# Kernel tuning notes

Hardware: AMD Instinct MI355X
Metric: run time of the kernel (lower is better)

The kernel has to match this reference:

```python
import jax, jax.numpy as jnp
import numpy as np

E = 512       # embed_dim
H = 8         # num_heads
DH = E // H   # head dim
F = 2048      # dim_feedforward
KS = 33       # NATTEN kernel_size (dilation=1)
NCLS = 1
B = 2
L = 4096      # local tokens (total seq = L + NCLS)
EPS = 1e-5


def layernorm(x, g, b):
    mu = jnp.mean(x, axis=-1, keepdims=True)
    var = jnp.mean(jnp.square(x - mu), axis=-1, keepdims=True)
    return (x - mu) * jax.lax.rsqrt(var + EPS) * g + b


def natten_1d(x, qkv_w, qkv_b, proj_w, proj_b):
    # Neighborhood attention 1D, dilation=1, non-causal, no rel-pos bias.
    b, l, e = x.shape
    qkv = x @ qkv_w.T + qkv_b                       # [b, l, 3E]
    q, k, v = jnp.split(qkv, 3, axis=-1)
    q = q.reshape(b, l, H, DH) * (DH ** -0.5)
    k = k.reshape(b, l, H, DH)
    v = v.reshape(b, l, H, DH)
    # NATTEN window: centered, shifted at edges to keep exactly KS in-bounds neighbors
    starts = jnp.clip(jnp.arange(l) - KS // 2, 0, l - KS)   # [l]
    idx = starts[:, None] + jnp.arange(KS)                  # [l, KS]
    kn = k[:, idx]                                          # [b, l, KS, H, DH]
    vn = v[:, idx]                                          # [b, l, KS, H, DH]
    attn = jnp.einsum('blhd,blkhd->bhlk', q, kn)
    attn = jax.nn.softmax(attn, axis=-1)
    out = jnp.einsum('bhlk,blkhd->blhd', attn, vn).reshape(b, l, e)
    return out @ proj_w.T + proj_b


def global_mha(q_in, kv_in, in_w, in_b, out_w, out_b):
    # torch nn.MultiheadAttention, batch_first, no masks
    bq, lq, e = q_in.shape
    lk = kv_in.shape[1]
    wq, wk, wv = jnp.split(in_w, 3, axis=0)
    bqp, bkp, bvp = jnp.split(in_b, 3, axis=0)
    q = (q_in @ wq.T + bqp).reshape(bq, lq, H, DH) * (DH ** -0.5)
    k = (kv_in @ wk.T + bkp).reshape(bq, lk, H, DH)
    v = (kv_in @ wv.T + bvp).reshape(bq, lk, H, DH)
    attn = jax.nn.softmax(jnp.einsum('bqhd,bkhd->bhqk', q, k), axis=-1)
    out = jnp.einsum('bhqk,bkhd->bqhd', attn, v).reshape(bq, lq, e)
    return out @ out_w.T + out_b


def setup_inputs() -> dict:
    key = jax.random.key(0)
    ks = jax.random.split(key, 16)
    s = 0.02
    return {
        'x': jax.random.normal(ks[0], (B, L + NCLS, E), jnp.float32),
        'ln1_g': jnp.ones((E,), jnp.float32),
        'ln1_b': jnp.zeros((E,), jnp.float32),
        'qkv_w': jax.random.normal(ks[1], (3 * E, E), jnp.float32) * s,
        'qkv_b': jnp.zeros((3 * E,), jnp.float32),
        'na_proj_w': jax.random.normal(ks[2], (E, E), jnp.float32) * s,
        'na_proj_b': jnp.zeros((E,), jnp.float32),
        'in_proj_w': jax.random.normal(ks[3], (3 * E, E), jnp.float32) * s,
        'in_proj_b': jnp.zeros((3 * E,), jnp.float32),
        'out_w': jax.random.normal(ks[4], (E, E), jnp.float32) * s,
        'out_b': jnp.zeros((E,), jnp.float32),
        'ln2_g': jnp.ones((E,), jnp.float32),
        'ln2_b': jnp.zeros((E,), jnp.float32),
        'fc1_w': jax.random.normal(ks[5], (F, E), jnp.float32) * s,
        'fc1_b': jnp.zeros((F,), jnp.float32),
        'fc2_w': jax.random.normal(ks[6], (E, F), jnp.float32) * s,
        'fc2_b': jnp.zeros((E,), jnp.float32),
    }


def reference(x, ln1_g, ln1_b, qkv_w, qkv_b, na_proj_w, na_proj_b,
              in_proj_w, in_proj_b, out_w, out_b, ln2_g, ln2_b,
              fc1_w, fc1_b, fc2_w, fc2_b):
    res = x
    xn = layernorm(x, ln1_g, ln1_b)
    x_local = natten_1d(xn[:, :-NCLS, :], qkv_w, qkv_b, na_proj_w, na_proj_b)
    tmp_key = jnp.concatenate([x_local, xn[:, -NCLS:, :]], axis=1)
    x_cls = global_mha(xn[:, -NCLS:, :], tmp_key, in_proj_w, in_proj_b, out_w, out_b)
    x = res + jnp.concatenate([x_local, x_cls], axis=1)
    res = x
    xn = layernorm(x, ln2_g, ln2_b)
    h = jax.nn.silu(xn @ fc1_w.T + fc1_b)
    return res + (h @ fc2_w.T + fc2_b)
```

## Files before the change

kernel.cpp:

```cpp
#include <hip/hip_runtime.h>
#include <hip/hip_bf16.h>
#include <cstdint>
#include <cstddef>

#define E    512
#define H    8
#define DHD  64
#define FDIM 2048
#define KS   33
#define BB   2
#define LL   4096
#define LP1  4097
#define NTOK 8194
#define NLOC 8192

typedef unsigned short ushort_t;
typedef __bf16 bf16x8_t __attribute__((ext_vector_type(8)));
typedef float  f32x4_t  __attribute__((ext_vector_type(4)));

__device__ __forceinline__ float b2f(unsigned short h) {
  union { unsigned int u; float f; } un; un.u = ((unsigned int)h) << 16; return un.f;
}
__device__ __forceinline__ unsigned short f2b(float f) {
  union { float f; unsigned int u; } un; un.f = f;
  unsigned int u = un.u;
  return (unsigned short)((u + 0x7FFFu + ((u >> 16) & 1u)) >> 16);
}

__device__ __forceinline__ void gload16(const ushort_t* g, ushort_t* l) {
  __builtin_amdgcn_global_load_lds(
      (const __attribute__((address_space(1))) void*)g,
      (__attribute__((address_space(3))) void*)l,
      16, 0, 0);
}

template<int N> __device__ __forceinline__ void waitcnt_vm() {
  if constexpr (N == 8)      asm volatile("s_waitcnt vmcnt(8)" ::: "memory");
  else if constexpr (N == 6) asm volatile("s_waitcnt vmcnt(6)" ::: "memory");
  else                       asm volatile("s_waitcnt vmcnt(0)" ::: "memory");
}

__device__ __forceinline__ int xcd_remap(int hw, int n) {
  int xcd = hw & 7, j = hw >> 3;
  int q = n >> 3, r = n & 7;
  return (xcd < r ? xcd * (q + 1) : r * (q + 1) + (xcd - r) * q) + j;
}

template<int BNT, int WC, int ACT, int OUTF, int ADDRES, int INRM, int OUTRM, int PARTIAL>
__global__ __launch_bounds__(256) void gemm_bt(
    const ushort_t* __restrict__ A, const ushort_t* __restrict__ W,
    const float* __restrict__ bias, float* __restrict__ outF,
    ushort_t* __restrict__ outB, const float* __restrict__ res,
    int M, int N, int K, int klen, int ny, int nz, size_t pstr)
{
  constexpr int MF  = 4;
  constexpr int NF  = BNT / (WC * 16);
  constexpr int BR  = (BNT * 64) / (8 * 256);
  constexpr int NLD = 4 + BR;
  __shared__ ushort_t Alds[2][128 * 64];
  __shared__ ushort_t Blds[2][BNT * 64];
  const int t    = threadIdx.x;
  const int lane = t & 63;
  const int w    = t >> 6;
  const int wr   = w / WC, wc = w % WC;

  const int Lid = xcd_remap(blockIdx.x, gridDim.x);
  const int bx  = Lid / (ny * nz);
  const int rem = Lid % (ny * nz);
  const int z   = rem / ny;
  const int by  = rem % ny;
  const int bmBase = bx * 128;
  const int bnBase = by * BNT;
  const int kbeg = z * klen;

  f32x4_t zero = {0.f, 0.f, 0.f, 0.f};
  f32x4_t acc[MF][NF];
  #pragma unroll
  for (int m = 0; m < MF; ++m)
    #pragma unroll
    for (int n = 0; n < NF; ++n) acc[m][n] = zero;

  const int srow = t >> 3;
  const int jsw8 = ((t & 7) ^ (srow & 7)) * 8;
  int arow[4];
  #pragma unroll
  for (int r = 0; r < 4; ++r) {
    int rr = bmBase + r * 32 + srow;
    if (INRM) rr += rr >> 12;
    else if (rr >= M) rr = M - 1;
    arow[r] = rr;
  }
  int brow[BR];
  #pragma unroll
  for (int r = 0; r < BR; ++r) brow[r] = bnBase + r * 32 + srow;

  const int frow = lane & 15;
  const int g    = lane >> 4;

  auto STAGE = [&](int s, int k0) {
    #pragma unroll
    for (int r = 0; r < 4; ++r)
      gload16(A + (size_t)arow[r] * K + k0 + jsw8, &Alds[s][(size_t)(r * 256 + t) * 8]);
    #pragma unroll
    for (int r = 0; r < BR; ++r)
      gload16(W + (size_t)brow[r] * K + k0 + jsw8, &Blds[s][(size_t)(r * 256 + t) * 8]);
  };

  const int nt = klen >> 6;
  STAGE(0, kbeg);
  if (nt > 1) STAGE(1, kbeg + 64);

  for (int it = 0; it < nt; ++it) {
    const int cur = it & 1;
    if (it < nt - 1) waitcnt_vm<NLD>();
    else             waitcnt_vm<0>();
    __builtin_amdgcn_s_barrier();
    #pragma unroll
    for (int kk2 = 0; kk2 < 2; ++kk2) {
      bf16x8_t af[MF], bfv[NF];
      const int kosw = ((kk2 * 4 + g) ^ (frow & 7)) << 4;
      #pragma unroll
      for (int m = 0; m < MF; ++m) {
        int row = wr * 64 + m * 16 + frow;
        af[m] = *reinterpret_cast<const bf16x8_t*>((char*)Alds[cur] + row * 128 + kosw);
      }
      #pragma unroll
      for (int n = 0; n < NF; ++n) {
        int row = wc * (BNT / WC) + n * 16 + frow;
        bfv[n] = *reinterpret_cast<const bf16x8_t*>((char*)Blds[cur] + row * 128 + kosw);
      }
      __builtin_amdgcn_s_setprio(1);
      #pragma unroll
      for (int m = 0; m < MF; ++m)
        #pragma unroll
        for (int n = 0; n < NF; ++n)
          acc[m][n] = __builtin_amdgcn_mfma_f32_16x16x32_bf16(af[m], bfv[n], acc[m][n], 0, 0, 0);
      __builtin_amdgcn_s_setprio(0);
    }
    __builtin_amdgcn_s_barrier();
    if (it + 2 < nt) STAGE(cur, kbeg + (it + 2) * 64);
  }

  const int rbase = g * 4;
  const int cbase = frow;
  float* po = nullptr;
  if (PARTIAL) po = (z == nz - 1) ? (float*)outB : outF + (size_t)z * pstr;
  #pragma unroll
  for (int m = 0; m < MF; ++m) {
    #pragma unroll
    for (int r = 0; r < 4; ++r) {
      int gr = bmBase + wr * 64 + m * 16 + rbase + r;
      if (gr < M) {
        int orow = OUTRM ? gr + (gr >> 12) : gr;
        #pragma unroll
        for (int n = 0; n < NF; ++n) {
          int gc = bnBase + wc * (BNT / WC) + n * 16 + cbase;
          float v = acc[m][n][r];
          if (PARTIAL) {
            po[(size_t)orow * N + gc] = v;
          } else {
            v += bias[gc];
            if (ACT == 1) v = v / (1.f + __expf(-v));
            if (ADDRES) v += res[(size_t)gr * N + gc];
            if (OUTF) outF[(size_t)orow * N + gc] = v;
            else      outB[(size_t)orow * N + gc] = f2b(v);
          }
        }
      }
    }
  }
}

template<int NP>
__global__ __launch_bounds__(256) void fc2_reduce(
    float* __restrict__ out, const float* __restrict__ parts, size_t pstr4,
    const float* __restrict__ bias, const float* __restrict__ xa)
{
  size_t i = (size_t)blockIdx.x * 256 + threadIdx.x;
  float4 o = reinterpret_cast<const float4*>(out)[i];
  float4 x = reinterpret_cast<const float4*>(xa)[i];
  float4 bcol = reinterpret_cast<const float4*>(bias)[i & 127];
  o.x += x.x + bcol.x; o.y += x.y + bcol.y;
  o.z += x.z + bcol.z; o.w += x.w + bcol.w;
  #pragma unroll
  for (int zp = 0; zp < NP - 1; ++zp) {
    float4 a = reinterpret_cast<const float4*>(parts)[zp * pstr4 + i];
    o.x += a.x; o.y += a.y; o.z += a.z; o.w += a.w;
  }
  reinterpret_cast<float4*>(out)[i] = o;
}

__global__ __launch_bounds__(256) void ln_fused1(
    const float* __restrict__ x, const float* __restrict__ g,
    const float* __restrict__ be, ushort_t* __restrict__ xn,
    ushort_t* __restrict__ tmpk)
{
  __shared__ float sh[4];
  const int row = blockIdx.x;
  const int t = threadIdx.x;
  const float* xr = x + (size_t)row * E;
  float v0 = xr[t], v1 = xr[t + 256];
  float sum = v0 + v1;
  #pragma unroll
  for (int o = 32; o; o >>= 1) sum += __shfl_xor(sum, o);
  if ((t & 63) == 0) sh[t >> 6] = sum;
  __syncthreads();
  float mean = (sh[0] + sh[1] + sh[2] + sh[3]) * (1.f / E);
  __syncthreads();
  float d0 = v0 - mean, d1 = v1 - mean;
  float vs = d0 * d0 + d1 * d1;
  #pragma unroll
  for (int o = 32; o; o >>= 1) vs += __shfl_xor(vs, o);
  if ((t & 63) == 0) sh[t >> 6] = vs;
  __syncthreads();
  float var = (sh[0] + sh[1] + sh[2] + sh[3]) * (1.f / E);
  float rstd = rsqrtf(var + 1e-5f);
  unsigned short o0 = f2b(d0 * rstd * g[t] + be[t]);
  unsigned short o1 = f2b(d1 * rstd * g[t + 256] + be[t + 256]);
  xn[(size_t)row * E + t] = o0;
  xn[(size_t)row * E + t + 256] = o1;
  if ((row % LP1) == LL) {
    tmpk[(size_t)row * E + t] = o0;
    tmpk[(size_t)row * E + t + 256] = o1;
  }
}

__global__ __launch_bounds__(256) void resid_ln2(
    const float* __restrict__ x, const ushort_t* __restrict__ tmpk,
    const float* __restrict__ xcls, const float* __restrict__ g,
    const float* __restrict__ be, float* __restrict__ xa,
    ushort_t* __restrict__ xn2)
{
  __shared__ float sh[4];
  const int row = blockIdx.x;
  const int b = row / LP1, l = row % LP1;
  const int t = threadIdx.x;
  float a0, a1;
  if (l < LL) { a0 = b2f(tmpk[(size_t)row * E + t]); a1 = b2f(tmpk[(size_t)row * E + t + 256]); }
  else        { a0 = xcls[b * E + t];                a1 = xcls[b * E + t + 256]; }
  float v0 = x[(size_t)row * E + t] + a0;
  float v1 = x[(size_t)row * E + t + 256] + a1;
  xa[(size_t)row * E + t] = v0;
  xa[(size_t)row * E + t + 256] = v1;
  float sum = v0 + v1;
  #pragma unroll
  for (int o = 32; o; o >>= 1) sum += __shfl_xor(sum, o);
  if ((t & 63) == 0) sh[t >> 6] = sum;
  __syncthreads();
  float mean = (sh[0] + sh[1] + sh[2] + sh[3]) * (1.f / E);
  __syncthreads();
  float d0 = v0 - mean, d1 = v1 - mean;
  float vs = d0 * d0 + d1 * d1;
  #pragma unroll
  for (int o = 32; o; o >>= 1) vs += __shfl_xor(vs, o);
  if ((t & 63) == 0) sh[t >> 6] = vs;
  __syncthreads();
  float var = (sh[0] + sh[1] + sh[2] + sh[3]) * (1.f / E);
  float rstd = rsqrtf(var + 1e-5f);
  xn2[(size_t)row * E + t]       = f2b(d0 * rstd * g[t] + be[t]);
  xn2[(size_t)row * E + t + 256] = f2b(d1 * rstd * g[t + 256] + be[t + 256]);
}

__global__ __launch_bounds__(256) void natten_mfma(
    const ushort_t* __restrict__ qkv, ushort_t* __restrict__ out)
{
  __shared__ ushort_t KP[4][64 * 64];
  __shared__ ushort_t VT[4][64 * 72];
  const int w    = threadIdx.x >> 6;
  const int lane = threadIdx.x & 63;
  const int task = blockIdx.x * 4 + w;
  const int h  = task & 7;
  const int qb = (task >> 3) & 127;
  const int b  = task >> 10;
  const int l0 = qb * 32;
  const int kb = l0 - 16;
  const ushort_t* base = qkv + (size_t)b * LL * (3 * E);
  ushort_t* Klds = KP[w];
  ushort_t* Vt   = VT[w];

  {
    const int rsub = lane >> 3;
    const int d0   = (lane & 7) * 8;
    #pragma unroll
    for (int i = 0; i < 8; ++i) {
      int row = i * 8 + rsub;
      int gl = kb + row; gl = gl < 0 ? 0 : (gl > LL - 1 ? LL - 1 : gl);
      bf16x8_t kv = *reinterpret_cast<const bf16x8_t*>(
          base + (size_t)gl * (3 * E) + E + h * 64 + d0);
      int ba = (row * 128 + d0 * 2) ^ ((row & 7) << 4);
      *reinterpret_cast<bf16x8_t*>((char*)Klds + ba) = kv;
    }
  }
  {
    const int a  = lane & 7;
    const int c8 = lane >> 3;
    unsigned int* Vt32 = (unsigned int*)Vt;
    #pragma unroll
    for (int i = 0; i < 4; ++i) {
      int rp = i * 8 + c8;
      int g0 = kb + rp * 2;     g0 = g0 < 0 ? 0 : (g0 > LL - 1 ? LL - 1 : g0);
      int g1 = kb + rp * 2 + 1; g1 = g1 < 0 ? 0 : (g1 > LL - 1 ? LL - 1 : g1);
      const ushort_t* v0 = base + (size_t)g0 * (3 * E) + 2 * E + h * 64 + a * 8;
      const ushort_t* v1 = base + (size_t)g1 * (3 * E) + 2 * E + h * 64 + a * 8;
      ushort4 x0 = *(const ushort4*)v0,       x1 = *(const ushort4*)v1;
      ushort4 y0 = *(const ushort4*)(v0 + 4), y1 = *(const ushort4*)(v1 + 4);
      int d = a * 8;
      Vt32[(d + 0) * 36 + rp] = (unsigned)x0.x | ((unsigned)x1.x << 16);
      Vt32[(d + 1) * 36 + rp] = (unsigned)x0.y | ((unsigned)x1.y << 16);
      Vt32[(d + 2) * 36 + rp] = (unsigned)x0.z | ((unsigned)x1.z << 16);
      Vt32[(d + 3) * 36 + rp] = (unsigned)x0.w | ((unsigned)x1.w << 16);
      Vt32[(d + 4) * 36 + rp] = (unsigned)y0.x | ((unsigned)y1.x << 16);
      Vt32[(d + 5) * 36 + rp] = (unsigned)y0.y | ((unsigned)y1.y << 16);
      Vt32[(d + 6) * 36 + rp] = (unsigned)y0.z | ((unsigned)y1.z << 16);
      Vt32[(d + 7) * 36 + rp] = (unsigned)y0.w | ((unsigned)y1.w << 16);
    }
  }

  const int p = lane & 15, g = lane >> 4;
  bf16x8_t qf[2][2];
  #pragma unroll
  for (int mt = 0; mt < 2; ++mt)
    #pragma unroll
    for (int ks = 0; ks < 2; ++ks)
      qf[mt][ks] = *reinterpret_cast<const bf16x8_t*>(
          base + (size_t)(l0 + mt * 16 + p) * (3 * E) + h * 64 + ks * 32 + g * 8);

  f32x4_t zero = {0.f, 0.f, 0.f, 0.f};
  f32x4_t accS[2][4];
  #pragma unroll
  for (int mt = 0; mt < 2; ++mt)
    #pragma unroll
    for (int nt = 0; nt < 4; ++nt) accS[mt][nt] = zero;
  #pragma unroll
  for (int ks = 0; ks < 2; ++ks) {
    bf16x8_t kf[4];
    #pragma unroll
    for (int nt = 0; nt < 4; ++nt) {
      int row = nt * 16 + p;
      int ba = (row * 128 + (ks * 32 + g * 8) * 2) ^ ((row & 7) << 4);
      kf[nt] = *reinterpret_cast<const bf16x8_t*>((char*)Klds + ba);
    }
    #pragma unroll
    for (int mt = 0; mt < 2; ++mt)
      #pragma unroll
      for (int nt = 0; nt < 4; ++nt)
        accS[mt][nt] = __builtin_amdgcn_mfma_f32_16x16x32_bf16(qf[mt][ks], kf[nt], accS[mt][nt], 0, 0, 0);
  }

  ushort_t* Plds = Klds;
  #pragma unroll
  for (int mt = 0; mt < 2; ++mt) {
    #pragma unroll
    for (int r = 0; r < 4; ++r) {
      int lq = l0 + mt * 16 + g * 4 + r;
      int st = lq - 16; st = st < 0 ? 0 : (st > LL - KS ? LL - KS : st);
      int clo = st - kb, chi = clo + 32;
      float sv[4];
      float mx = -1e30f;
      #pragma unroll
      for (int nt = 0; nt < 4; ++nt) {
        int c = nt * 16 + p;
        float s = accS[mt][nt][r] * 0.125f;
        s = (c >= clo && c <= chi) ? s : -1e30f;
        sv[nt] = s;
        mx = fmaxf(mx, s);
      }
      mx = fmaxf(mx, __shfl_xor(mx, 1));
      mx = fmaxf(mx, __shfl_xor(mx, 2));
      mx = fmaxf(mx, __shfl_xor(mx, 4));
      mx = fmaxf(mx, __shfl_xor(mx, 8));
      float sum = 0.f;
      #pragma unroll
      for (int nt = 0; nt < 4; ++nt) { float e = __expf(sv[nt] - mx); sv[nt] = e; sum += e; }
      sum += __shfl_xor(sum, 1);
      sum += __shfl_xor(sum, 2);
      sum += __shfl_xor(sum, 4);
      sum += __shfl_xor(sum, 8);
      float inv = 1.f / sum;
      int q = mt * 16 + g * 4 + r;
      #pragma unroll
      for (int nt = 0; nt < 4; ++nt)
        Plds[q * 72 + nt * 16 + p] = f2b(sv[nt] * inv);
    }
  }

  f32x4_t accO[2][4];
  #pragma unroll
  for (int mt = 0; mt < 2; ++mt)
    #pragma unroll
    for (int nt = 0; nt < 4; ++nt) accO[mt][nt] = zero;
  #pragma unroll
  for (int ks = 0; ks < 2; ++ks) {
    bf16x8_t pf[2], vf[4];
    #pragma unroll
    for (int mt = 0; mt < 2; ++mt)
      pf[mt] = *reinterpret_cast<const bf16x8_t*>(
          (char*)Plds + (mt * 16 + p) * 144 + (ks * 32 + g * 8) * 2);
    #pragma unroll
    for (int nt = 0; nt < 4; ++nt)
      vf[nt] = *reinterpret_cast<const bf16x8_t*>(
          (char*)Vt + (nt * 16 + p) * 144 + (ks * 32 + g * 8) * 2);
    #pragma unroll
    for (int mt = 0; mt < 2; ++mt)
      #pragma unroll
      for (int nt = 0; nt < 4; ++nt)
        accO[mt][nt] = __builtin_amdgcn_mfma_f32_16x16x32_bf16(pf[mt], vf[nt], accO[mt][nt], 0, 0, 0);
  }

  #pragma unroll
  for (int mt = 0; mt < 2; ++mt) {
    #pragma unroll
    for (int r = 0; r < 4; ++r) {
      int lq = l0 + mt * 16 + g * 4 + r;
      ushort_t* orow = out + ((size_t)(b * LL) + lq) * E + h * 64;
      #pragma unroll
      for (int nt = 0; nt < 4; ++nt)
        orow[nt * 16 + p] = f2b(accO[mt][nt][r]);
    }
  }
}

__global__ __launch_bounds__(256) void qcls_kernel(
    const ushort_t* __restrict__ xn, const float* __restrict__ inw,
    const float* __restrict__ inb, float* __restrict__ qcls)
{
  int i = blockIdx.x * 256 + threadIdx.x;
  int b = i >> 9, d = i & 511;
  const ushort_t* xr = xn + ((size_t)b * LP1 + LL) * E;
  const float* wr = inw + (size_t)d * E;
  float s = 0.f;
  for (int e = 0; e < E; e += 4) {
    ushort4 xv = *reinterpret_cast<const ushort4*>(xr + e);
    s += b2f(xv.x) * wr[e] + b2f(xv.y) * wr[e + 1] + b2f(xv.z) * wr[e + 2] + b2f(xv.w) * wr[e + 3];
  }
  qcls[i] = (s + inb[d]) * 0.125f;
}

__global__ __launch_bounds__(256) void gscore_kernel(
    const float* __restrict__ qcls, const ushort_t* __restrict__ kv,
    float* __restrict__ sc)
{
  const int wav = blockIdx.x * 4 + (threadIdx.x >> 6);
  if (wav >= BB * LP1) return;
  const int lane = threadIdx.x & 63;
  const int b = wav / LP1, j = wav % LP1;
  const ushort_t* kr = kv + (size_t)wav * 1024 + lane * 8;
  const float* q = qcls + b * E + lane * 8;
  ushort4 ka = *reinterpret_cast<const ushort4*>(kr);
  ushort4 kb4 = *reinterpret_cast<const ushort4*>(kr + 4);
  float s = b2f(ka.x) * q[0] + b2f(ka.y) * q[1] + b2f(ka.z) * q[2] + b2f(ka.w) * q[3]
          + b2f(kb4.x) * q[4] + b2f(kb4.y) * q[5] + b2f(kb4.z) * q[6] + b2f(kb4.w) * q[7];
  s += __shfl_xor(s, 1); s += __shfl_xor(s, 2); s += __shfl_xor(s, 4);
  if ((lane & 7) == 0) sc[((size_t)(b * 8) + (lane >> 3)) * LP1 + j] = s;
}

__global__ __launch_bounds__(256) void gsoftmax_kernel(float* __restrict__ sc)
{
  float* row = sc + (size_t)blockIdx.x * LP1;
  __shared__ float sh[4];
  const int t = threadIdx.x;
  float m = -1e30f;
  for (int i = t; i < LP1; i += 256) m = fmaxf(m, row[i]);
  #pragma unroll
  for (int o = 32; o; o >>= 1) m = fmaxf(m, __shfl_xor(m, o));
  if ((t & 63) == 0) sh[t >> 6] = m;
  __syncthreads();
  m = fmaxf(fmaxf(sh[0], sh[1]), fmaxf(sh[2], sh[3]));
  __syncthreads();
  float s = 0.f;
  for (int i = t; i < LP1; i += 256) { float e = __expf(row[i] - m); row[i] = e; s += e; }
  #pragma unroll
  for (int o = 32; o; o >>= 1) s += __shfl_xor(s, o);
  if ((t & 63) == 0) sh[t >> 6] = s;
  __syncthreads();
  float inv = 1.f / (sh[0] + sh[1] + sh[2] + sh[3]);
  for (int i = t; i < LP1; i += 256) row[i] *= inv;
}

__global__ __launch_bounds__(256) void gpv_kernel(
    const float* __restrict__ sc, const ushort_t* __restrict__ kv,
    float* __restrict__ parts)
{
  __shared__ float red[4][64];
  const int bh = blockIdx.y;
  const int b = bh >> 3, h = bh & 7;
  const int c = blockIdx.x;
  const int lane = threadIdx.x & 63, s4 = threadIdx.x >> 6;
  const int j0 = c * 512;
  const int jend = (j0 + 512 < LP1) ? j0 + 512 : LP1;
  const float* prow = sc + (size_t)bh * LP1;
  const ushort_t* vbase = kv + (size_t)b * LP1 * 1024 + 512 + h * 64 + lane;
  float acc = 0.f;
  for (int j = j0 + s4; j < jend; j += 4)
    acc += prow[j] * b2f(vbase[(size_t)j * 1024]);
  red[s4][lane] = acc;
  __syncthreads();
  if (s4 == 0)
    parts[((size_t)c * 16 + bh) * 64 + lane] = red[0][lane] + red[1][lane] + red[2][lane] + red[3][lane];
}

__global__ void gpv_reduce(const float* __restrict__ parts, float* __restrict__ oc)
{
  int i = blockIdx.x * 256 + threadIdx.x;
  if (i < BB * E) {
    float s = 0.f;
    #pragma unroll
    for (int c = 0; c < 9; ++c) s += parts[c * 1024 + i];
    oc[i] = s;
  }
}

__global__ __launch_bounds__(256) void xcls_kernel(
    const float* __restrict__ oc, const float* __restrict__ ow,
    const float* __restrict__ ob, float* __restrict__ xc)
{
  int i = blockIdx.x * 256 + threadIdx.x;
  if (i >= BB * E) return;
  int b = i >> 9, n = i & 511;
  const float* o = oc + b * E;
  const float* wr = ow + (size_t)n * E;
  float s = ob[n];
  for (int m = 0; m < E; ++m) s += o[m] * wr[m];
  xc[i] = s;
}

__global__ void cvt_all(
    const float* __restrict__ s0, ushort_t* __restrict__ d0, int n0,
    const float* __restrict__ s1, ushort_t* __restrict__ d1, int n1,
    const float* __restrict__ s2, ushort_t* __restrict__ d2, int n2,
    const float* __restrict__ s3, ushort_t* __restrict__ d3, int n3,
    const float* __restrict__ s4, ushort_t* __restrict__ d4, int n4)
{
  int i = (blockIdx.x * 256 + threadIdx.x) * 4;
  const float* s; ushort_t* d;
  if (i < n0)                { s = s0; d = d0; }
  else if ((i -= n0) < n1)   { s = s1; d = d1; }
  else if ((i -= n1) < n2)   { s = s2; d = d2; }
  else if ((i -= n2) < n3)   { s = s3; d = d3; }
  else if ((i -= n3) < n4)   { s = s4; d = d4; }
  else return;
  float4 v = *reinterpret_cast<const float4*>(s + i);
  ushort4 o;
  o.x = f2b(v.x); o.y = f2b(v.y); o.z = f2b(v.z); o.w = f2b(v.w);
  *reinterpret_cast<ushort4*>(d + i) = o;
}

extern "C" void kernel_launch(void* const* d_in, const int* in_sizes, int n_in,
                              void* d_out, int out_size, void* d_ws, size_t ws_size,
                              hipStream_t stream)
{
  const float* x      = (const float*)d_in[0];
  const float* ln1_g  = (const float*)d_in[1];
  const float* ln1_b  = (const float*)d_in[2];
  const float* qkv_w  = (const float*)d_in[3];
  const float* qkv_b  = (const float*)d_in[4];
  const float* na_w   = (const float*)d_in[5];
  const float* na_b   = (const float*)d_in[6];
  const float* in_w   = (const float*)d_in[7];
  const float* in_b   = (const float*)d_in[8];
  const float* out_w  = (const float*)d_in[9];
  const float* out_b  = (const float*)d_in[10];
  const float* ln2_g  = (const float*)d_in[11];
  const float* ln2_b  = (const float*)d_in[12];
  const float* fc1_w  = (const float*)d_in[13];
  const float* fc1_b  = (const float*)d_in[14];
  const float* fc2_w  = (const float*)d_in[15];
  const float* fc2_b  = (const float*)d_in[16];
  float* out = (float*)d_out;

  char* pws = (char*)d_ws;
  size_t off = 0;
  auto alloc = [&](size_t bytes) {
    void* r = pws + off; off = (off + bytes + 255) & ~(size_t)255; return r;
  };
  ushort_t* w_qkv = (ushort_t*)alloc((size_t)3 * E * E * 2);
  ushort_t* w_na  = (ushort_t*)alloc((size_t)E * E * 2);
  ushort_t* w_in  = (ushort_t*)alloc((size_t)3 * E * E * 2);
  ushort_t* w_fc1 = (ushort_t*)alloc((size_t)FDIM * E * 2);
  ushort_t* w_fc2 = (ushort_t*)alloc((size_t)E * FDIM * 2);
  ushort_t* xn1   = (ushort_t*)alloc((size_t)NTOK * E * 2);
  char*     bigR  = (char*)alloc((size_t)NTOK * FDIM * 2);
  ushort_t* qkvb  = (ushort_t*)bigR;
  ushort_t* natt  = (ushort_t*)(bigR + (size_t)NLOC * 3 * E * 2);
  ushort_t* kvg   = (ushort_t*)bigR;
  ushort_t* hbuf  = (ushort_t*)bigR;
  ushort_t* tmpk  = (ushort_t*)alloc((size_t)NTOK * E * 2);
  float*    sc    = (float*)alloc((size_t)BB * H * LP1 * 4);
  float*    qcls  = (float*)alloc(1024 * 4);
  float*    parts = (float*)alloc(9 * 16 * 64 * 4);
  float*    oc    = (float*)alloc(1024 * 4);
  float*    xcls  = (float*)alloc(1024 * 4);
  float*    xa    = (float*)alloc((size_t)NTOK * E * 4);
  ushort_t* xn2   = xn1;
  const size_t PS = (size_t)NTOK * E;
  size_t off_save = off;
  float* sk = (float*)alloc(3 * PS * 4);
  int nsplit = 4;
  if (off > ws_size) {
    off = off_save;
    sk = (float*)alloc(PS * 4);
    nsplit = 2;
    if (off > ws_size) { off = off_save; nsplit = 1; }
  }

  cvt_all<<<3840, 256, 0, stream>>>(
      qkv_w, w_qkv, 3 * E * E,
      na_w,  w_na,  E * E,
      in_w,  w_in,  3 * E * E,
      fc1_w, w_fc1, FDIM * E,
      fc2_w, w_fc2, E * FDIM);

  ln_fused1<<<NTOK, 256, 0, stream>>>(x, ln1_g, ln1_b, xn1, tmpk);
  qcls_kernel<<<4, 256, 0, stream>>>(xn1, in_w, in_b, qcls);
  gemm_bt<128,2, 0,0,0,1,0,0><<<64 * 12, 256, 0, stream>>>(
      xn1, w_qkv, qkv_b, nullptr, qkvb, nullptr, NLOC, 3 * E, E, E, 12, 1, 0);
  natten_mfma<<<512, 256, 0, stream>>>(qkvb, natt);
  gemm_bt<64,2, 0,0,0,0,1,0><<<64 * 8, 256, 0, stream>>>(
      natt, w_na, na_b, nullptr, tmpk, nullptr, NLOC, E, E, E, 8, 1, 0);
  gemm_bt<128,2, 0,0,0,0,0,0><<<65 * 8, 256, 0, stream>>>(
      tmpk, w_in + (size_t)E * E, in_b + E, nullptr, kvg, nullptr, NTOK, 1024, E, E, 8, 1, 0);
  gscore_kernel<<<(BB * LP1 + 3) / 4, 256, 0, stream>>>(qcls, kvg, sc);
  gsoftmax_kernel<<<BB * H, 256, 0, stream>>>(sc);
  gpv_kernel<<<dim3(9, BB * H), 256, 0, stream>>>(sc, kvg, parts);
  gpv_reduce<<<4, 256, 0, stream>>>(parts, oc);
  xcls_kernel<<<4, 256, 0, stream>>>(oc, out_w, out_b, xcls);
  resid_ln2<<<NTOK, 256, 0, stream>>>(x, tmpk, xcls, ln2_g, ln2_b, xa, xn2);
  gemm_bt<128,2, 1,0,0,0,0,0><<<65 * 16, 256, 0, stream>>>(
      xn2, w_fc1, fc1_b, nullptr, hbuf, nullptr, NTOK, FDIM, E, E, 16, 1, 0);
  if (nsplit == 4) {
    gemm_bt<128,2, 0,0,0,0,0,1><<<65 * 4 * 4, 256, 0, stream>>>(
        hbuf, w_fc2, fc2_b, sk, (ushort_t*)out, nullptr, NTOK, E, FDIM, FDIM / 4, 4, 4, PS);
    fc2_reduce<4><<<(NTOK * E / 4) / 256, 256, 0, stream>>>(out, sk, PS / 4, fc2_b, xa);
  } else if (nsplit == 2) {
    gemm_bt<128,2, 0,0,0,0,0,1><<<65 * 4 * 2, 256, 0, stream>>>(
        hbuf, w_fc2, fc2_b, sk, (ushort_t*)out, nullptr, NTOK, E, FDIM, FDIM / 2, 4, 2, PS);
    fc2_reduce<2><<<(NTOK * E / 4) / 256, 256, 0, stream>>>(out, sk, PS / 4, fc2_b, xa);
  } else {
    gemm_bt<128,2, 0,1,1,0,0,0><<<65 * 4, 256, 0, stream>>>(
        hbuf, w_fc2, fc2_b, out, nullptr, xa, NTOK, E, FDIM, FDIM, 4, 1, 0);
  }
}
```

Baseline: 282.4 us.

## Generalize GEMM tile shape, use bf16 partials and residual buffers

The GEMM kernel is templated on M-tile and thread count, and the QKV, FC1 and FC2 GEMMs move to 256-row tiles run by 512-thread blocks. The split-K FC2 partials and the residual buffer are now stored as bf16 instead of fp32, which halves their memory traffic, and every split goes through the reduce kernel. The s_setprio hints around the MFMA loop are also removed. Rounding the residual and the partial sums to bf16 lowers accuracy, and the larger tiles mean fewer blocks with more registers and LDS per block.

New measurement: 292.8 us. 3.7% more time.

```diff
diff --git a/kernel.cpp b/kernel.cpp
--- a/kernel.cpp
+++ b/kernel.cpp
@@ -46,18 +46,22 @@
   return (xcd < r ? xcd * (q + 1) : r * (q + 1) + (xcd - r) * q) + j;
 }
 
-template<int BNT, int WC, int ACT, int OUTF, int ADDRES, int INRM, int OUTRM, int PARTIAL>
-__global__ __launch_bounds__(256) void gemm_bt(
+template<int BMT, int BNT, int NTH, int WC, int ACT, int OUTF, int ADDRES,
+         int INRM, int OUTRM, int PARTIAL>
+__global__ __launch_bounds__(NTH) void gemm_bt(
     const ushort_t* __restrict__ A, const ushort_t* __restrict__ W,
     const float* __restrict__ bias, float* __restrict__ outF,
-    ushort_t* __restrict__ outB, const float* __restrict__ res,
+    ushort_t* __restrict__ outB, const ushort_t* __restrict__ res,
     int M, int N, int K, int klen, int ny, int nz, size_t pstr)
 {
-  constexpr int MF  = 4;
+  constexpr int WR  = NTH / 64 / WC;
+  constexpr int MF  = BMT / (WR * 16);
   constexpr int NF  = BNT / (WC * 16);
-  constexpr int BR  = (BNT * 64) / (8 * 256);
-  constexpr int NLD = 4 + BR;
-  __shared__ ushort_t Alds[2][128 * 64];
+  constexpr int AR  = (BMT * 64) / (8 * NTH);
+  constexpr int BR  = (BNT * 64) / (8 * NTH);
+  constexpr int RPR = NTH / 8;
+  constexpr int NLD = AR + BR;
+  __shared__ ushort_t Alds[2][BMT * 64];
   __shared__ ushort_t Blds[2][BNT * 64];
   const int t    = threadIdx.x;
   const int lane = t & 63;
@@ -69,7 +73,7 @@
   const int rem = Lid % (ny * nz);
   const int z   = rem / ny;
   const int by  = rem % ny;
-  const int bmBase = bx * 128;
+  const int bmBase = bx * BMT;
   const int bnBase = by * BNT;
   const int kbeg = z * klen;
 
@@ -82,28 +86,28 @@
 
   const int srow = t >> 3;
   const int jsw8 = ((t & 7) ^ (srow & 7)) * 8;
-  int arow[4];
-  #pragma unroll
-  for (int r = 0; r < 4; ++r) {
-    int rr = bmBase + r * 32 + srow;
+  int arow[AR];
+  #pragma unroll
+  for (int r = 0; r < AR; ++r) {
+    int rr = bmBase + r * RPR + srow;
     if (INRM) rr += rr >> 12;
     else if (rr >= M) rr = M - 1;
     arow[r] = rr;
   }
   int brow[BR];
   #pragma unroll
-  for (int r = 0; r < BR; ++r) brow[r] = bnBase + r * 32 + srow;
+  for (int r = 0; r < BR; ++r) brow[r] = bnBase + r * RPR + srow;
 
   const int frow = lane & 15;
   const int g    = lane >> 4;
 
   auto STAGE = [&](int s, int k0) {
     #pragma unroll
-    for (int r = 0; r < 4; ++r)
-      gload16(A + (size_t)arow[r] * K + k0 + jsw8, &Alds[s][(size_t)(r * 256 + t) * 8]);
+    for (int r = 0; r < AR; ++r)
+      gload16(A + (size_t)arow[r] * K + k0 + jsw8, &Alds[s][(size_t)(r * NTH + t) * 8]);
     #pragma unroll
     for (int r = 0; r < BR; ++r)
-      gload16(W + (size_t)brow[r] * K + k0 + jsw8, &Blds[s][(size_t)(r * 256 + t) * 8]);
+      gload16(W + (size_t)brow[r] * K + k0 + jsw8, &Blds[s][(size_t)(r * NTH + t) * 8]);
   };
 
   const int nt = klen >> 6;
@@ -121,21 +125,19 @@
       const int kosw = ((kk2 * 4 + g) ^ (frow & 7)) << 4;
       #pragma unroll
       for (int m = 0; m < MF; ++m) {
-        int row = wr * 64 + m * 16 + frow;
+        int row = wr * (MF * 16) + m * 16 + frow;
         af[m] = *reinterpret_cast<const bf16x8_t*>((char*)Alds[cur] + row * 128 + kosw);
       }
       #pragma unroll
       for (int n = 0; n < NF; ++n) {
-        int row = wc * (BNT / WC) + n * 16 + frow;
+        int row = wc * (NF * 16) + n * 16 + frow;
         bfv[n] = *reinterpret_cast<const bf16x8_t*>((char*)Blds[cur] + row * 128 + kosw);
       }
-      __builtin_amdgcn_s_setprio(1);
       #pragma unroll
       for (int m = 0; m < MF; ++m)
         #pragma unroll
         for (int n = 0; n < NF; ++n)
           acc[m][n] = __builtin_amdgcn_mfma_f32_16x16x32_bf16(af[m], bfv[n], acc[m][n], 0, 0, 0);
-      __builtin_amdgcn_s_setprio(0);
     }
     __builtin_amdgcn_s_barrier();
     if (it + 2 < nt) STAGE(cur, kbeg + (it + 2) * 64);
@@ -143,25 +145,23 @@
 
   const int rbase = g * 4;
   const int cbase = frow;
-  float* po = nullptr;
-  if (PARTIAL) po = (z == nz - 1) ? (float*)outB : outF + (size_t)z * pstr;
   #pragma unroll
   for (int m = 0; m < MF; ++m) {
     #pragma unroll
     for (int r = 0; r < 4; ++r) {
-      int gr = bmBase + wr * 64 + m * 16 + rbase + r;
+      int gr = bmBase + wr * (MF * 16) + m * 16 + rbase + r;
       if (gr < M) {
         int orow = OUTRM ? gr + (gr >> 12) : gr;
         #pragma unroll
         for (int n = 0; n < NF; ++n) {
-          int gc = bnBase + wc * (BNT / WC) + n * 16 + cbase;
+          int gc = bnBase + wc * (NF * 16) + n * 16 + cbase;
           float v = acc[m][n][r];
           if (PARTIAL) {
-            po[(size_t)orow * N + gc] = v;
+            outB[(size_t)z * pstr + (size_t)orow * N + gc] = f2b(v);
           } else {
             v += bias[gc];
             if (ACT == 1) v = v / (1.f + __expf(-v));
-            if (ADDRES) v += res[(size_t)gr * N + gc];
+            if (ADDRES) v += b2f(res[(size_t)gr * N + gc]);
             if (OUTF) outF[(size_t)orow * N + gc] = v;
             else      outB[(size_t)orow * N + gc] = f2b(v);
           }
@@ -173,21 +173,21 @@
 
 template<int NP>
 __global__ __launch_bounds__(256) void fc2_reduce(
-    float* __restrict__ out, const float* __restrict__ parts, size_t pstr4,
-    const float* __restrict__ bias, const float* __restrict__ xa)
-{
-  size_t i = (size_t)blockIdx.x * 256 + threadIdx.x;
-  float4 o = reinterpret_cast<const float4*>(out)[i];
-  float4 x = reinterpret_cast<const float4*>(xa)[i];
-  float4 bcol = reinterpret_cast<const float4*>(bias)[i & 127];
-  o.x += x.x + bcol.x; o.y += x.y + bcol.y;
-  o.z += x.z + bcol.z; o.w += x.w + bcol.w;
-  #pragma unroll
-  for (int zp = 0; zp < NP - 1; ++zp) {
-    float4 a = reinterpret_cast<const float4*>(parts)[zp * pstr4 + i];
-    o.x += a.x; o.y += a.y; o.z += a.z; o.w += a.w;
-  }
-  reinterpret_cast<float4*>(out)[i] = o;
+    float* __restrict__ out, const ushort_t* __restrict__ parts, size_t pstr,
+    const float* __restrict__ bias, const ushort_t* __restrict__ xab)
+{
+  size_t i4 = (size_t)blockIdx.x * 256 + threadIdx.x;
+  ushort4 xv = reinterpret_cast<const ushort4*>(xab)[i4];
+  float4 bcol = reinterpret_cast<const float4*>(bias)[i4 & 127];
+  float4 o;
+  o.x = b2f(xv.x) + bcol.x; o.y = b2f(xv.y) + bcol.y;
+  o.z = b2f(xv.z) + bcol.z; o.w = b2f(xv.w) + bcol.w;
+  #pragma unroll
+  for (int zp = 0; zp < NP; ++zp) {
+    ushort4 pv = *reinterpret_cast<const ushort4*>(parts + (size_t)zp * pstr + i4 * 4);
+    o.x += b2f(pv.x); o.y += b2f(pv.y); o.z += b2f(pv.z); o.w += b2f(pv.w);
+  }
+  reinterpret_cast<float4*>(out)[i4] = o;
 }
 
 __global__ __launch_bounds__(256) void ln_fused1(
@@ -228,7 +228,7 @@
 __global__ __launch_bounds__(256) void resid_ln2(
     const float* __restrict__ x, const ushort_t* __restrict__ tmpk,
     const float* __restrict__ xcls, const float* __restrict__ g,
-    const float* __restrict__ be, float* __restrict__ xa,
+    const float* __restrict__ be, ushort_t* __restrict__ xab,
     ushort_t* __restrict__ xn2)
 {
   __shared__ float sh[4];
@@ -240,8 +240,8 @@
   else        { a0 = xcls[b * E + t];                a1 = xcls[b * E + t + 256]; }
   float v0 = x[(size_t)row * E + t] + a0;
   float v1 = x[(size_t)row * E + t + 256] + a1;
-  xa[(size_t)row * E + t] = v0;
-  xa[(size_t)row * E + t + 256] = v1;
+  xab[(size_t)row * E + t] = f2b(v0);
+  xab[(size_t)row * E + t + 256] = f2b(v1);
   float sum = v0 + v1;
   #pragma unroll
   for (int o = 32; o; o >>= 1) sum += __shfl_xor(sum, o);
@@ -590,15 +590,15 @@
   float*    parts = (float*)alloc(9 * 16 * 64 * 4);
   float*    oc    = (float*)alloc(1024 * 4);
   float*    xcls  = (float*)alloc(1024 * 4);
-  float*    xa    = (float*)alloc((size_t)NTOK * E * 4);
+  ushort_t* xab   = (ushort_t*)alloc((size_t)NTOK * E * 2);
   ushort_t* xn2   = xn1;
   const size_t PS = (size_t)NTOK * E;
   size_t off_save = off;
-  float* sk = (float*)alloc(3 * PS * 4);
+  ushort_t* sk = (ushort_t*)alloc(4 * PS * 2);
   int nsplit = 4;
   if (off > ws_size) {
     off = off_save;
-    sk = (float*)alloc(PS * 4);
+    sk = (ushort_t*)alloc(2 * PS * 2);
     nsplit = 2;
     if (off > ws_size) { off = off_save; nsplit = 1; }
   }
@@ -612,31 +612,31 @@
 
   ln_fused1<<<NTOK, 256, 0, stream>>>(x, ln1_g, ln1_b, xn1, tmpk);
   qcls_kernel<<<4, 256, 0, stream>>>(xn1, in_w, in_b, qcls);
-  gemm_bt<128,2, 0,0,0,1,0,0><<<64 * 12, 256, 0, stream>>>(
-      xn1, w_qkv, qkv_b, nullptr, qkvb, nullptr, NLOC, 3 * E, E, E, 12, 1, 0);
+  gemm_bt<256,256,512,4, 0,0,0,1,0,0><<<192, 512, 0, stream>>>(
+      xn1, w_qkv, qkv_b, nullptr, qkvb, nullptr, NLOC, 3 * E, E, E, 6, 1, 0);
   natten_mfma<<<512, 256, 0, stream>>>(qkvb, natt);
-  gemm_bt<64,2, 0,0,0,0,1,0><<<64 * 8, 256, 0, stream>>>(
+  gemm_bt<128,64,256,2, 0,0,0,0,1,0><<<512, 256, 0, stream>>>(
       natt, w_na, na_b, nullptr, tmpk, nullptr, NLOC, E, E, E, 8, 1, 0);
-  gemm_bt<128,2, 0,0,0,0,0,0><<<65 * 8, 256, 0, stream>>>(
+  gemm_bt<128,128,256,2, 0,0,0,0,0,0><<<520, 256, 0, stream>>>(
       tmpk, w_in + (size_t)E * E, in_b + E, nullptr, kvg, nullptr, NTOK, 1024, E, E, 8, 1, 0);
   gscore_kernel<<<(BB * LP1 + 3) / 4, 256, 0, stream>>>(qcls, kvg, sc);
   gsoftmax_kernel<<<BB * H, 256, 0, stream>>>(sc);
   gpv_kernel<<<dim3(9, BB * H), 256, 0, stream>>>(sc, kvg, parts);
   gpv_reduce<<<4, 256, 0, stream>>>(parts, oc);
   xcls_kernel<<<4, 256, 0, stream>>>(oc, out_w, out_b, xcls);
-  resid_ln2<<<NTOK, 256, 0, stream>>>(x, tmpk, xcls, ln2_g, ln2_b, xa, xn2);
-  gemm_bt<128,2, 1,0,0,0,0,0><<<65 * 16, 256, 0, stream>>>(
+  resid_ln2<<<NTOK, 256, 0, stream>>>(x, tmpk, xcls, ln2_g, ln2_b, xab, xn2);
+  gemm_bt<256,128,512,4, 1,0,0,0,0,0><<<528, 512, 0, stream>>>(
       xn2, w_fc1, fc1_b, nullptr, hbuf, nullptr, NTOK, FDIM, E, E, 16, 1, 0);
   if (nsplit == 4) {
-    gemm_bt<128,2, 0,0,0,0,0,1><<<65 * 4 * 4, 256, 0, stream>>>(
-        hbuf, w_fc2, fc2_b, sk, (ushort_t*)out, nullptr, NTOK, E, FDIM, FDIM / 4, 4, 4, PS);
-    fc2_reduce<4><<<(NTOK * E / 4) / 256, 256, 0, stream>>>(out, sk, PS / 4, fc2_b, xa);
+    gemm_bt<256,128,512,4, 0,0,0,0,0,1><<<528, 512, 0, stream>>>(
+        hbuf, w_fc2, fc2_b, nullptr, sk, nullptr, NTOK, E, FDIM, FDIM / 4, 4, 4, PS);
+    fc2_reduce<4><<<(NTOK * E / 4) / 256, 256, 0, stream>>>(out, sk, PS, fc2_b, xab);
   } else if (nsplit == 2) {
-    gemm_bt<128,2, 0,0,0,0,0,1><<<65 * 4 * 2, 256, 0, stream>>>(
-        hbuf, w_fc2, fc2_b, sk, (ushort_t*)out, nullptr, NTOK, E, FDIM, FDIM / 2, 4, 2, PS);
-    fc2_reduce<2><<<(NTOK * E / 4) / 256, 256, 0, stream>>>(out, sk, PS / 4, fc2_b, xa);
+    gemm_bt<256,128,512,4, 0,0,0,0,0,1><<<33 * 4 * 2, 512, 0, stream>>>(
+        hbuf, w_fc2, fc2_b, nullptr, sk, nullptr, NTOK, E, FDIM, FDIM / 2, 4, 2, PS);
+    fc2_reduce<2><<<(NTOK * E / 4) / 256, 256, 0, stream>>>(out, sk, PS, fc2_b, xab);
   } else {
-    gemm_bt<128,2, 0,1,1,0,0,0><<<65 * 4, 256, 0, stream>>>(
-        hbuf, w_fc2, fc2_b, out, nullptr, xa, NTOK, E, FDIM, FDIM, 4, 1, 0);
-  }
-}
+    gemm_bt<256,128,512,4, 0,1,1,0,0,0><<<33 * 4, 512, 0, stream>>>(
+        hbuf, w_fc2, fc2_b, out, nullptr, xab, NTOK, E, FDIM, FDIM, 4, 1, 0);
+  }
+}
```
